# Performance work log

Hardware: AMD Instinct MI355X
Metric: run time of the kernel (lower is better)

The kernel has to match this reference:

```python
import jax, jax.numpy as jnp
import numpy as np

B = 4
N_SAMPLES = 32768
N_EVENTS = 32
N_HARMONICS = 16
SAMPLES_PER_FRAME = 256
N_FRAMES = N_SAMPLES // SAMPLES_PER_FRAME  # 128
SAMPLERATE = 22050
NYQ = SAMPLERATE // 2
MIN_F = 20.0 / NYQ
MAX_F = 4000.0 / NYQ
RES_BASE = 0.8
N_ROOMS = 8
LOG_SQRT_2PI = 0.5 * np.log(2.0 * np.pi).astype(np.float32)


def max_norm(x):
    return x / (jnp.max(jnp.abs(x), axis=-1, keepdims=True) + 1e-8)


def window(means, stds, n, mn, mx, eps=1e-8):
    # means/stds: [B, E, 1]; Normal pdf evaluated on linspace(0,1,n), max-normalized
    mu = mn + means * (mx - mn)
    sigma = eps + stds
    rng = jnp.linspace(0.0, 1.0, n, dtype=jnp.float32)[None, None, :]
    logp = -0.5 * ((rng - mu) / sigma) ** 2 - jnp.log(sigma) - LOG_SQRT_2PI
    return max_norm(jnp.exp(logp))


def interp_linear(x, out_size):
    # F.interpolate(mode='linear', align_corners=False) along last axis
    in_size = x.shape[-1]
    coords = (jnp.arange(out_size, dtype=jnp.float32) + 0.5) * (in_size / out_size) - 0.5
    coords = jnp.clip(coords, 0.0, in_size - 1.0)
    lo = jnp.floor(coords).astype(jnp.int32)
    hi = jnp.minimum(lo + 1, in_size - 1)
    w = (coords - lo.astype(jnp.float32))
    return x[..., lo] * (1.0 - w) + x[..., hi] * w


def fft_convolve(a, b):
    # zero-padded linear convolution via FFT, truncated to original length
    n = a.shape[-1]
    pa = jnp.pad(a, [(0, 0)] * (a.ndim - 1) + [(0, n)])
    pb = jnp.pad(b, [(0, 0)] * (b.ndim - 1) + [(0, n)])
    out = jnp.fft.irfft(jnp.fft.rfft(pa) * jnp.fft.rfft(pb), n=2 * n)
    return out[..., :n]


def setup_inputs():
    key = jax.random.key(0)
    k1, k2, k3, k4, k5 = jax.random.split(key, 5)
    return {
        'event_params': jax.random.uniform(k1, (B, N_EVENTS, N_HARMONICS + 6), dtype=jnp.float32),
        'mx_raw': jax.random.normal(k2, (B,), dtype=jnp.float32),
        'room_logits': jax.random.normal(k3, (B, N_ROOMS), dtype=jnp.float32),
        'noise': jax.random.uniform(k4, (1, 1, N_SAMPLES), dtype=jnp.float32, minval=-1.0, maxval=1.0),
        'impulse_responses': jax.random.normal(k5, (N_ROOMS, N_SAMPLES), dtype=jnp.float32) * 0.01,
    }


def reference(event_params, mx_raw, room_logits, noise, impulse_responses):
    b = event_params.shape[0]
    ep = event_params  # [B, E, 22], already in [0,1] (post-activation)
    freq_means = ep[:, :, 0:1] ** 2
    freq_stds = ep[:, :, 1:2] * 0.1
    time_means = ep[:, :, 2:3]
    time_stds = ep[:, :, 3:4] * 0.1
    f0 = ep[:, :, 4:5] ** 2
    amps = ep[:, :, 5:6] ** 2
    res = ep[:, :, 6:] * (1.0 - RES_BASE) + RES_BASE  # [B, E, H]
    mx = jax.nn.sigmoid(mx_raw).reshape(b, 1, 1)
    rooms = jax.nn.softmax(room_logits, axis=-1)

    # --- BandLimitedNoise ---
    nfft = N_SAMPLES // 2 + 1
    win = window(freq_means, freq_stds, nfft, MIN_F, MAX_F)  # [B, E, nfft]
    noise_spec = jnp.fft.rfft(noise, norm='ortho')            # [1, 1, nfft]
    bl_noise = jnp.fft.irfft(noise_spec * win, n=N_SAMPLES, norm='ortho')  # [B, E, N]

    # --- impulse (time) windows ---
    events = window(time_means, time_stds, N_SAMPLES, 0.0, 1.0)  # [B, E, N]

    # --- Resonance ---
    factors = jnp.arange(1, N_HARMONICS + 1, dtype=jnp.float32)
    f0s = MIN_F + (MAX_F - MIN_F) * f0                 # [B, E, 1]
    freqs = f0s * factors                               # [B, E, H]
    freqs = jnp.where(freqs >= 1.0, 0.0, freqs)
    freqs_fr = jnp.broadcast_to(freqs[..., None], freqs.shape + (N_FRAMES,))
    freqs_s = interp_linear(freqs_fr, N_SAMPLES)        # [B, E, H, N]
    res_fr = jnp.cumprod(jnp.broadcast_to(res[..., None], res.shape + (N_FRAMES,)), axis=-1)
    res_s = interp_linear(res_fr, N_SAMPLES)            # [B, E, H, N]
    resonances = jnp.sum(res_s * jnp.sin(jnp.cumsum(freqs_s * (2.0 * np.pi), axis=-1)), axis=2)  # [B, E, N]

    # --- locate events + resonance convolution (noise_coeff = 1) ---
    located = bl_noise * events * amps
    located = fft_convolve(located, resonances) + located
    located = jnp.sum(located, axis=1, keepdims=True)   # [B, 1, N]

    # --- reverb: rooms-weighted impulse response, dry/wet mix ---
    dry = located
    imp = jnp.einsum('br,rn->bn', rooms, impulse_responses)[:, None, :]
    wet = fft_convolve(located, imp)
    return dry * (1.0 - mx) + wet * mx
```

## Files before the change

kernel.cpp:

```cpp
#include <hip/hip_runtime.h>
#include <math.h>

#define NSAMP 32768
#define NPAD  65536
#define NCH   128
#define TWO_PI 6.2831853071795864f
#define MINF ((float)(20.0/11025.0))
#define DRF  ((float)(4000.0/11025.0 - 20.0/11025.0))

__device__ __forceinline__ float2 cxmul(float2 a, float2 b){
    return make_float2(a.x*b.x - a.y*b.y, a.x*b.y + a.y*b.x);
}

template<int DIR>
__device__ __forceinline__ void fft4v(float2* v, int i0, int i1, int i2, int i3){
    float2 a=v[i0], b=v[i1], c=v[i2], d=v[i3];
    float2 t0 = make_float2(a.x+c.x, a.y+c.y);
    float2 t1 = make_float2(a.x-c.x, a.y-c.y);
    float2 t2 = make_float2(b.x+d.x, b.y+d.y);
    float2 t3 = make_float2(b.x-d.x, b.y-d.y);
    v[i0] = make_float2(t0.x+t2.x, t0.y+t2.y);
    v[i2] = make_float2(t0.x-t2.x, t0.y-t2.y);
    if (DIR < 0) {
        v[i1] = make_float2(t1.x + t3.y, t1.y - t3.x);
        v[i3] = make_float2(t1.x - t3.y, t1.y + t3.x);
    } else {
        v[i1] = make_float2(t1.x - t3.y, t1.y + t3.x);
        v[i3] = make_float2(t1.x + t3.y, t1.y - t3.x);
    }
}

template<int DIR>
__device__ __forceinline__ void twm(float2& v, float c, float s){
    float sy = (DIR<0) ? -s : s;
    v = cxmul(v, make_float2(c, sy));
}

template<int DIR>
__device__ __forceinline__ void fft16r(float2* v){
    const float C1=0.92387953251128674f, S1=0.38268343236508978f, H=0.70710678118654752f;
    fft4v<DIR>(v,0,4,8,12);
    fft4v<DIR>(v,1,5,9,13);
    fft4v<DIR>(v,2,6,10,14);
    fft4v<DIR>(v,3,7,11,15);
    twm<DIR>(v[5],  C1, S1);
    twm<DIR>(v[6],  H,  H);
    twm<DIR>(v[7],  S1, C1);
    twm<DIR>(v[9],  H,  H);
    twm<DIR>(v[10], 0.0f, 1.0f);
    twm<DIR>(v[11], -H, H);
    twm<DIR>(v[13], S1, C1);
    twm<DIR>(v[14], -H, H);
    twm<DIR>(v[15], -C1, -S1);
    fft4v<DIR>(v,0,1,2,3);
    fft4v<DIR>(v,4,5,6,7);
    fft4v<DIR>(v,8,9,10,11);
    fft4v<DIR>(v,12,13,14,15);
}

template<int DIR>
__device__ __forceinline__ void fft8r(float2* v){
    const float H=0.70710678118654752f;
    #pragma unroll
    for (int n1=0;n1<4;n1++){
        float2 t=v[n1], u=v[n1+4];
        v[n1]   = make_float2(t.x+u.x, t.y+u.y);
        v[n1+4] = make_float2(t.x-u.x, t.y-u.y);
    }
    twm<DIR>(v[5], H, H);
    twm<DIR>(v[6], 0.0f, 1.0f);
    twm<DIR>(v[7], -H, H);
    fft4v<DIR>(v,0,1,2,3);
    fft4v<DIR>(v,4,5,6,7);
}

__device__ __forceinline__ int slot16(int r){ return ((r&3)<<2)|(r>>2); }
__device__ __forceinline__ int slot8(int r){ return ((r&1)<<2)|(r>>1); }
__device__ __forceinline__ int lxs(int l){ return l ^ ((l>>4)&15); }

template<int R>
__device__ __forceinline__ void twiddle(float2* v, float ang1){
    float s,c; __sincosf(ang1,&s,&c);
    float2 w[R];
    w[1] = make_float2(c,s);
    #pragma unroll
    for (int r=2;r<R;r++) w[r] = cxmul(w[r>>1], w[r-(r>>1)]);
    #pragma unroll
    for (int r=1;r<R;r++) v[r] = cxmul(v[r], w[r]);
}

template<int DIR>
__device__ __forceinline__ void n1_tail(float2 (&v)[16], float2* lds, int t, int p,
                                        float2* __restrict__ out)
{
    fft16r<DIR>(v);
    #pragma unroll
    for (int r=0;r<16;r++) lds[lxs(256*(t>>4) + 16*(t&15) + r)] = v[slot16(r)];
    __syncthreads();
    #pragma unroll
    for (int q=0;q<16;q++) v[q] = lds[lxs(256*q + t)];
    int jm = t & 15;
    if (jm) twiddle<16>(v, (DIR<0?-TWO_PI:TWO_PI)*(float)jm*(1.0f/256.0f));
    fft16r<DIR>(v);
    int j2 = 256*p + t;
    float2* yo = out + (j2>>4)*256 + (j2&15);
    #pragma unroll
    for (int r=0;r<16;r++) yo[16*r] = v[slot16(r)];
}

__global__ __launch_bounds__(256) void mfk_n1_noise_setup(const float* __restrict__ noise,
        float2* __restrict__ dst, const float* __restrict__ EP,
        const float* __restrict__ MXR, const float* __restrict__ RL,
        float* __restrict__ chP, unsigned* __restrict__ chQ, float* __restrict__ chR,
        float* __restrict__ cum, float* __restrict__ mxA, float* __restrict__ rmA)
{
    __shared__ float2 lds[4096];
    int t = threadIdx.x, px = blockIdx.x;
    if (px >= 8){
        int q = (px-8)*256 + t;
        int c = q >> 4, h = q & 15;
        const float* P = EP + c*22;
        const float LSQ = (float)0.9189385332046727;
        float f0m = __fmul_rn(P[4],P[4]);
        float f0s = __fadd_rn(MINF, __fmul_rn(f0m, DRF));
        float fr  = __fmul_rn(f0s, (float)(h+1));
        if (fr >= 1.0f) fr = 0.0f;
        chQ[q] = (unsigned)(unsigned long long)((double)fr*4294967296.0 + 0.5);
        float rs = __fadd_rn(__fmul_rn(P[6+h],0.2f),0.8f);
        chR[q] = rs;
        float cp = rs;
        float* crow = cum + (size_t)q*128;
        for (int jj=0;jj<128;jj++){ crow[jj] = cp; cp = __fmul_rn(cp, rs); }
        if (h == 0){
            float fm  = __fmul_rn(P[0],P[0]);
            float fmu = __fadd_rn(MINF, __fmul_rn(fm, DRF));
            float fsg = 1e-8f + P[1]*0.1f;
            float fsi = 1.0f/fsg;
            int i0 = (int)floorf(fmu*16384.0f + 0.5f);
            i0 = min(max(i0,0),16384);
            float rg = (float)i0 * (1.0f/16384.0f);
            float tt = (rg - fmu)*fsi;
            float Lc = logf(fsg) + LSQ;
            float sc = expf(-Lc) / (expf(-0.5f*tt*tt - Lc) + 1e-8f);
            float tmu = P[2];
            float tsg = 1e-8f + P[3]*0.1f;
            float tsi = 1.0f/tsg;
            int i1 = (int)floorf(tmu*32767.0f + 0.5f);
            i1 = min(max(i1,0),32767);
            float rg1 = (float)((double)i1 * (1.0/32767.0));
            float tt1 = (rg1 - tmu)*tsi;
            float Lc1 = logf(tsg) + LSQ;
            float sc1 = expf(-Lc1) / (expf(-0.5f*tt1*tt1 - Lc1) + 1e-8f);
            float amp = P[5]*P[5];
            float* o = chP + c*8;
            o[0]=fmu; o[1]=fsi; o[2]=sc; o[3]=tmu; o[4]=tsi; o[5]=sc1; o[6]=amp; o[7]=0.f;
        }
        if (q < 4){
            int b = q;
            mxA[b] = 1.0f/(1.0f + expf(-MXR[b]));
            const float* rl = RL + b*8;
            float mx = rl[0];
            for (int r=1;r<8;r++) mx = fmaxf(mx, rl[r]);
            float sum=0.f;
            float e2[8];
            for (int r=0;r<8;r++){ e2[r]=expf(rl[r]-mx); sum+=e2[r]; }
            for (int r=0;r<8;r++) rmA[b*8+r] = e2[r]/sum;
        }
        return;
    }
    int p = px;
    int j = 128*(t>>4) + 16*p + (t&15);
    float2 v[16];
    #pragma unroll
    for (int r=0;r<16;r++) v[r] = make_float2(noise[j + 2048*r], 0.0f);
    n1_tail<-1>(v, lds, t, p, dst);
}

__global__ __launch_bounds__(256) void mfk_n1_specwin(const float2* __restrict__ nspec,
        const float* __restrict__ chP, float2* __restrict__ dst, int g0)
{
    __shared__ float2 lds[4096];
    int t = threadIdx.x, p = blockIdx.x, pr = blockIdx.y;
    int c0 = g0 + 2*pr;
    const float* A = chP + c0*8;
    const float* B = chP + (c0+1)*8;
    float a0=A[0], a1=A[1], a2=A[2], b0=B[0], b1=B[1], b2=B[2];
    int j = 128*(t>>4) + 16*p + (t&15);
    float2 v[16];
    #pragma unroll
    for (int r=0;r<16;r++){
        int k = j + 2048*r;
        int kw = (k <= 16384) ? k : (32768 - k);
        float rg = (float)kw * (1.0f/16384.0f);
        float t0 = (rg - a0)*a1;
        float w0 = expf(-0.5f*t0*t0)*a2;
        float t1 = (rg - b0)*b1;
        float w1 = expf(-0.5f*t1*t1)*b2;
        float2 N = nspec[k];
        v[r] = make_float2(N.x*w0 - N.y*w1, N.y*w0 + N.x*w1);
    }
    n1_tail<1>(v, lds, t, p, dst + (size_t)pr*NSAMP);
}

template<int DIR>
__device__ __forceinline__ void n2_stageC(const float2* __restrict__ x, float2* lds, int t, int p)
{
    float2 v[16];
    int j2 = 256*(t>>5) + 32*p + (t&31);
    #pragma unroll
    for (int r=0;r<16;r++) v[r] = x[j2 + 2048*r];
    int jm = 32*p + (t&31);
    if (jm) twiddle<16>(v, (DIR<0?-TWO_PI:TWO_PI)*(float)jm*(1.0f/4096.0f));
    fft16r<DIR>(v);
    #pragma unroll
    for (int r=0;r<16;r++) lds[lxs(256*r + t)] = v[slot16(r)];
    __syncthreads();
}

template<int DIR>
__device__ __forceinline__ int n2_stageD(float2* lds, int t, int p, int u, float2 (&w8)[8])
{
    int q = t + 256*u;
    int j3 = ((q>>5)<<8) + 32*p + (q&31);
    #pragma unroll
    for (int r3=0;r3<8;r3++) w8[r3] = lds[lxs(256*(q>>5) + 32*r3 + (q&31))];
    if (j3) twiddle<8>(w8, (DIR<0?-TWO_PI:TWO_PI)*(float)j3*(1.0f/32768.0f));
    fft8r<DIR>(w8);
    return j3;
}

__global__ __launch_bounds__(256) void mfk_n2_noise(const float2* __restrict__ src,
                                                    float2* __restrict__ dst)
{
    __shared__ float2 lds[4096];
    int t = threadIdx.x, p = blockIdx.x;
    n2_stageC<-1>(src, lds, t, p);
    #pragma unroll
    for (int u=0;u<2;u++){
        float2 w8[8];
        int j3 = n2_stageD<-1>(lds, t, p, u, w8);
        #pragma unroll
        for (int r=0;r<8;r++) dst[j3 + 4096*r] = w8[slot8(r)];
    }
}

__global__ __launch_bounds__(256) void mfk_n2_unpack(const float2* __restrict__ src,
        const float* __restrict__ chP, float* __restrict__ locraw, int g0)
{
    __shared__ float2 lds[4096];
    int t = threadIdx.x, p = blockIdx.x, pr = blockIdx.y;
    n2_stageC<1>(src + (size_t)pr*NSAMP, lds, t, p);
    int lc0 = 2*pr;
    const float* C0 = chP + (g0+lc0)*8;
    const float* C1 = chP + (g0+lc0+1)*8;
    float c03=C0[3], c04=C0[4], c05=C0[5], c06=C0[6];
    float c13=C1[3], c14=C1[4], c15=C1[5], c16=C1[6];
    #pragma unroll
    for (int u=0;u<2;u++){
        float2 w8[8];
        int j3 = n2_stageD<1>(lds, t, p, u, w8);
        #pragma unroll
        for (int r=0;r<8;r++){
            int n = j3 + 4096*r;
            float2 val = w8[slot8(r)];
            float rg = (float)((double)n * (1.0/32767.0));
            float tt0 = (rg - c03)*c04;
            float ew0 = expf(-0.5f*tt0*tt0)*c05;
            float tt1 = (rg - c13)*c14;
            float ew1 = expf(-0.5f*tt1*tt1)*c15;
            locraw[(size_t)lc0*NSAMP + n]     = val.x*(1.0f/32768.0f)*ew0*c06;
            locraw[(size_t)(lc0+1)*NSAMP + n] = val.y*(1.0f/32768.0f)*ew1*c16;
        }
    }
}

__global__ __launch_bounds__(256) void mfk_packZres_f01(const float* __restrict__ locraw,
        const unsigned* __restrict__ chQ, const float* __restrict__ chR,
        const float* __restrict__ cum, float2* __restrict__ dst, int g0)
{
    __shared__ float2 lds[4096];
    float* cumS = (float*)lds;
    unsigned* qS = (unsigned*)(cumS + 2048);
    float* rS = cumS + 2064;
    int t = threadIdx.x, p = blockIdx.x, lc = blockIdx.y;
    int cg = g0 + lc;
    const float* crow = cum + (size_t)cg*2048;
    #pragma unroll
    for (int i=0;i<8;i++) cumS[t + 256*i] = crow[t + 256*i];
    if (t < 16){ qS[t] = chQ[cg*16 + t]; rS[t] = chR[cg*16 + t]; }
    __syncthreads();
    int j = 256*(t>>4) + 16*p + (t&15);
    float co0 = ((float)j + 0.5f)*0.00390625f - 0.5f;
    float fl = floorf(co0);
    float wf = co0 - fl;
    int ilo = (int)fl;
    float acc[8];
    #pragma unroll
    for (int r=0;r<8;r++) acc[r] = 0.0f;
    if (j == 0) acc[0] = 1.0f;
    unsigned T1 = (unsigned)(j+1);
    #pragma unroll
    for (int hh=0; hh<16; hh++){
        unsigned qq = qS[hh];
        float rs = rS[hh];
        float rs2 = rs*rs, rs4 = rs2*rs2, rs8 = rs4*rs4, rs16 = rs8*rs8;
        float mix = fmaf(rs - 1.0f, wf, 1.0f);
        const float* cr = cumS + hh*128;
        unsigned bits = qq * T1;
        unsigned step = qq << 12;
        float e_cur = (ilo >= 0) ? cr[ilo] : cr[15];
        float env0  = (ilo >= 0) ? 0.0f : cr[0];
        #pragma unroll
        for (int r=0;r<8;r++){
            float env;
            if (r == 0 && ilo < 0) env = env0;
            else env = (ilo == 15 && r == 7) ? e_cur : e_cur*mix;
            float m = (float)bits * 2.3283064365386963e-10f;
            float sv; asm("v_sin_f32 %0, %1" : "=v"(sv) : "v"(m));
            acc[r] = fmaf(env, sv, acc[r]);
            bits += step;
            if (!(r == 0 && ilo < 0)) e_cur *= rs16;
        }
    }
    const float* la = locraw + (size_t)lc*NSAMP;
    float2 v[16];
    #pragma unroll
    for (int r=0;r<8;r++) v[r] = make_float2(la[j + 4096*r], acc[r]);
    #pragma unroll
    for (int r=8;r<16;r++) v[r] = make_float2(0.f,0.f);
    __syncthreads();
    n1_tail<-1>(v, lds, t, p, dst + (size_t)lc*NPAD);
}

template<int DIR, int NSTORE>
__global__ __launch_bounds__(256) void mfk_f23(const float2* __restrict__ src,
                                               float2* __restrict__ dst)
{
    __shared__ float2 lds[4096];
    int t = threadIdx.x, p = blockIdx.x;
    size_t boff = (size_t)blockIdx.y * NPAD;
    int a = t>>4, w = t&15;
    int j = 256*a + 16*p + w;
    const float2* x = src + boff;
    float2 v[16];
    #pragma unroll
    for (int r=0;r<16;r++) v[r] = x[j + 4096*r];
    int jm = 16*p + w;
    if (jm) twiddle<16>(v, (DIR<0?-TWO_PI:TWO_PI)*(float)jm*(1.0f/4096.0f));
    fft16r<DIR>(v);
    #pragma unroll
    for (int r=0;r<16;r++) lds[lxs(256*a + 16*r + w)] = v[slot16(r)];
    __syncthreads();
    #pragma unroll
    for (int q=0;q<16;q++) v[q] = lds[lxs(256*q + t)];
    if (j) twiddle<16>(v, (DIR<0?-TWO_PI:TWO_PI)*(float)j*(1.0f/65536.0f));
    fft16r<DIR>(v);
    float2* yo = dst + boff + j;
    #pragma unroll
    for (int r=0;r<NSTORE;r++) yo[4096*r] = v[slot16(r)];
}

__global__ __launch_bounds__(256) void mfk_prodacc(const float2* __restrict__ Z,
        float2* __restrict__ T, int g0, int G, int addTo)
{
    int x = blockIdx.x;
    int beta = blockIdx.y;
    int z = blockIdx.z;
    int g = ((x>>4)<<3) | (x&7);
    int kb = (x&8) ? (255 - g) : g;
    int k = kb*256 + threadIdx.x;
    int km = (NPAD - k) & (NPAD-1);
    int cstart = max(64*beta + 32*z, g0);
    int cend   = min(64*beta + 32*z + 32, g0+G);
    float2 S0 = make_float2(0.f,0.f), S1 = make_float2(0.f,0.f);
    #pragma unroll 4
    for (int c=cstart; c<cend; ++c){
        const float2* zp = Z + (size_t)(c-g0)*NPAD;
        float2 a = zp[k], am = zp[km];
        float2 A0 = make_float2(0.5f*(a.x+am.x), 0.5f*(a.y-am.y));
        float2 R0 = make_float2(0.5f*(a.y+am.y), -0.5f*(a.x-am.x));
        float2 P = cxmul(A0,R0);
        if ((c>>5)&1){ S1.x += P.x; S1.y += P.y; }
        else         { S0.x += P.x; S0.y += P.y; }
    }
    const float s = 1.0f/65536.0f;
    float2 q = make_float2((S0.x - S1.y)*s, (S0.y + S1.x)*s);
    size_t idx = ((size_t)z*2 + beta)*NPAD + k;
    if (addTo){ float2 o = T[idx]; q.x += o.x; q.y += o.y; }
    T[idx] = q;
}

__global__ __launch_bounds__(256) void mfk_plain_f01(const float2* __restrict__ T,
        float2* __restrict__ dst)
{
    __shared__ float2 lds[4096];
    int t = threadIdx.x, p = blockIdx.x, b = blockIdx.y;
    const float2* x0 = T + (size_t)b*NPAD;
    const float2* x1 = T + (size_t)(2+b)*NPAD;
    int j = 256*(t>>4) + 16*p + (t&15);
    float2 v[16];
    #pragma unroll
    for (int r=0;r<16;r++){
        float2 u0 = x0[j + 4096*r], u1 = x1[j + 4096*r];
        v[r] = make_float2(u0.x+u1.x, u0.y+u1.y);
    }
    n1_tail<1>(v, lds, t, p, dst + (size_t)b*NPAD);
}

__global__ __launch_bounds__(256) void mfk_dry_f01(const float2* __restrict__ U2,
        const float* __restrict__ rmA, const float* __restrict__ IR, float2* __restrict__ dst)
{
    __shared__ float2 lds[4096];
    int t = threadIdx.x, p = blockIdx.x, b = blockIdx.y;
    int j = 256*(t>>4) + 16*p + (t&15);
    float rm[8];
    #pragma unroll
    for (int r=0;r<8;r++) rm[r] = rmA[b*8+r];
    const float2* Ub = U2 + (size_t)(b>>1)*NPAD;
    float2 v[16];
    #pragma unroll
    for (int r=0;r<8;r++){
        int n = j + 4096*r;
        float2 lcv = Ub[n];
        float locv = (b&1) ? lcv.y : lcv.x;
        float iv = 0.f;
        #pragma unroll
        for (int q=0;q<8;q++) iv += rm[q]*IR[(size_t)q*NSAMP + n];
        v[r] = make_float2(locv, iv);
    }
    #pragma unroll
    for (int r=8;r<16;r++) v[r] = make_float2(0.f,0.f);
    n1_tail<-1>(v, lds, t, p, dst + (size_t)b*NPAD);
}

__global__ __launch_bounds__(256) void mfk_prod_f01(const float2* __restrict__ Z,
        float2* __restrict__ dst)
{
    __shared__ float2 lds[4096];
    int t = threadIdx.x;
    int px = blockIdx.x;
    int p = (px < 8) ? px : 23 - px;
    int pr = blockIdx.y;
    const float2* z0 = Z + (size_t)(2*pr)*NPAD;
    const float2* z1 = z0 + NPAD;
    int j = 256*(t>>4) + 16*p + (t&15);
    float2 v[16];
    #pragma unroll
    for (int r=0;r<16;r++){
        int k = j + 4096*r;
        int km = (NPAD - k) & (NPAD-1);
        float2 a = z0[k], am = z0[km];
        float2 A0 = make_float2(0.5f*(a.x+am.x), 0.5f*(a.y-am.y));
        float2 R0 = make_float2(0.5f*(a.y+am.y), -0.5f*(a.x-am.x));
        float2 P0 = cxmul(A0,R0);
        float2 b = z1[k], bm = z1[km];
        float2 A1 = make_float2(0.5f*(b.x+bm.x), 0.5f*(b.y-bm.y));
        float2 R1 = make_float2(0.5f*(b.y+bm.y), -0.5f*(b.x-bm.x));
        float2 P1 = cxmul(A1,R1);
        const float s = 1.0f/65536.0f;
        v[r] = make_float2((P0.x - P1.y)*s, (P0.y + P1.x)*s);
    }
    n1_tail<1>(v, lds, t, p, dst + (size_t)pr*NPAD);
}

__global__ __launch_bounds__(256) void mfk_f23_final(const float2* __restrict__ src,
        const float2* __restrict__ U2, const float* __restrict__ mxA,
        float* __restrict__ out)
{
    __shared__ float2 lds[4096];
    int t = threadIdx.x, p = blockIdx.x;
    int pr = blockIdx.y;
    size_t boff = (size_t)pr * NPAD;
    int a = t>>4, w = t&15;
    int j = 256*a + 16*p + w;
    const float2* x = src + boff;
    float2 v[16];
    #pragma unroll
    for (int r=0;r<16;r++) v[r] = x[j + 4096*r];
    int jm = 16*p + w;
    if (jm) twiddle<16>(v, TWO_PI*(float)jm*(1.0f/4096.0f));
    fft16r<1>(v);
    #pragma unroll
    for (int r=0;r<16;r++) lds[lxs(256*a + 16*r + w)] = v[slot16(r)];
    __syncthreads();
    #pragma unroll
    for (int q=0;q<16;q++) v[q] = lds[lxs(256*q + t)];
    if (j) twiddle<16>(v, TWO_PI*(float)j*(1.0f/65536.0f));
    fft16r<1>(v);
    int b0 = 2*pr, b1 = b0+1;
    float mx0 = mxA[b0], mx1 = mxA[b1];
    const float2* Ub = U2 + (size_t)pr*NPAD;
    #pragma unroll
    for (int r=0;r<8;r++){
        int ts = j + 4096*r;
        float2 val = v[slot16(r)];
        float2 dry = Ub[ts];
        out[(size_t)b0*NSAMP+ts] = dry.x*(1.f-mx0) + val.x*mx0;
        out[(size_t)b1*NSAMP+ts] = dry.y*(1.f-mx1) + val.y*mx1;
    }
}

extern "C" void kernel_launch(void* const* d_in, const int* in_sizes, int n_in,
                              void* d_out, int out_size, void* d_ws, size_t ws_size,
                              hipStream_t stream)
{
    (void)in_sizes; (void)n_in; (void)out_size;
    const float* EP   = (const float*)d_in[0];
    const float* MXR  = (const float*)d_in[1];
    const float* RL   = (const float*)d_in[2];
    const float* NOISE= (const float*)d_in[3];
    const float* IR   = (const float*)d_in[4];
    float* out = (float*)d_out;
    char* w = (char*)d_ws;

    auto need = [](long long g)->long long {
        return 2LL*g*NPAD*8 + 1LL*g*NSAMP*4 + (long long)NSAMP*8
             + 2048LL*128*4 + (128LL*8 + 2048 + 2048 + 4 + 32)*4
             + 4LL*NPAD*8  + 2LL*NPAD*8  + 16384;
    };
    int G = 128;
    while (G > 4 && need(G) > (long long)ws_size) G >>= 1;

    size_t off = 0;
    auto alloc = [&](size_t bytes)->char* {
        char* p = w + off; off += (bytes + 255) & ~(size_t)255; return p;
    };
    float2*   arA    = (float2*)alloc((size_t)G*NPAD*8);
    float2*   arB    = (float2*)alloc((size_t)G*NPAD*8);
    float*    locraw = (float*) alloc((size_t)G*NSAMP*4);
    float2*   T      = (float2*)alloc(4LL*NPAD*8);
    float2*   U2     = (float2*)alloc(2LL*NPAD*8);
    float2*   nspec  = (float2*)alloc((size_t)NSAMP*8);
    float*    cum    = (float*) alloc(2048LL*128*4);
    float*    chP    = (float*) alloc(128*8*4);
    unsigned* chQ    = (unsigned*)alloc(2048*4);
    float*    chR    = (float*) alloc(2048*4);
    float*    mxA    = (float*) alloc(4*4);
    float*    rmA    = (float*) alloc(32*4);

    mfk_n1_noise_setup<<<dim3(16),256,0,stream>>>(NOISE, arB, EP, MXR, RL,
                                                  chP, chQ, chR, cum, mxA, rmA);
    mfk_n2_noise<<<dim3(8),256,0,stream>>>(arB, nspec);

    for (int g0 = 0; g0 < NCH; g0 += G){
        int P = G/2;
        mfk_n1_specwin<<<dim3(8,P),256,0,stream>>>(nspec, chP, arA, g0);
        mfk_n2_unpack<<<dim3(8,P),256,0,stream>>>(arA, chP, locraw, g0);
        mfk_packZres_f01<<<dim3(16,G),256,0,stream>>>(locraw, chQ, chR, cum, arA, g0);
        mfk_f23<-1,16><<<dim3(16,G),256,0,stream>>>(arA, arB);
        mfk_prodacc<<<dim3(256,2,2),256,0,stream>>>(arB, T, g0, G, (g0>0)?1:0);
    }

    mfk_plain_f01<<<dim3(16,2),256,0,stream>>>(T, arB);
    mfk_f23<1,8><<<dim3(16,2),256,0,stream>>>(arB, U2);

    mfk_dry_f01<<<dim3(16,4),256,0,stream>>>(U2, rmA, IR, arA);
    mfk_f23<-1,16><<<dim3(16,4),256,0,stream>>>(arA, arB);
    mfk_prod_f01<<<dim3(16,2),256,0,stream>>>(arB, arA);
    mfk_f23_final<<<dim3(16,2),256,0,stream>>>(arA, U2, mxA, out);
}
```

Before: 176.3 us.

## Fold impulse-response FFT into event-batch FFT launches and shrink reverb tail

The room-weighted impulse responses are now built and forward-transformed as two extra rows in the per-chunk pack/FFT launches, instead of in a separate tail stage. The reverb tail then forward-transforms only the two packed located signals and multiplies them against the precomputed IR spectra, halving the tail FFT grid. This moves serial tail work into an already wide launch to shorten the critical path. In exchange, workspace grows by two rows, and if G is smaller than the channel count the IR rows are recomputed in every chunk.

```diff
diff --git a/kernel.cpp b/kernel.cpp
--- a/kernel.cpp
+++ b/kernel.cpp
@@ -276,20 +276,44 @@
 
 __global__ __launch_bounds__(256) void mfk_packZres_f01(const float* __restrict__ locraw,
         const unsigned* __restrict__ chQ, const float* __restrict__ chR,
-        const float* __restrict__ cum, float2* __restrict__ dst, int g0)
-{
-    __shared__ float2 lds[4096];
+        const float* __restrict__ cum, const float* __restrict__ rmA,
+        const float* __restrict__ IR, float2* __restrict__ dst, int g0, int nev)
+{
+    __shared__ float2 lds[4096];
+    int t = threadIdx.x, p = blockIdx.x, lc = blockIdx.y;
+    int j = 256*(t>>4) + 16*p + (t&15);
+    if (lc >= nev){
+        int pi = lc - nev;
+        float rm0[8], rm1[8];
+        #pragma unroll
+        for (int q=0;q<8;q++){ rm0[q] = rmA[(2*pi)*8+q]; rm1[q] = rmA[(2*pi+1)*8+q]; }
+        float2 v[16];
+        #pragma unroll
+        for (int r=0;r<8;r++){
+            int n = j + 4096*r;
+            float i0 = 0.f, i1 = 0.f;
+            #pragma unroll
+            for (int q=0;q<8;q++){
+                float ir = IR[(size_t)q*NSAMP + n];
+                i0 = fmaf(rm0[q], ir, i0);
+                i1 = fmaf(rm1[q], ir, i1);
+            }
+            v[r] = make_float2(i0, i1);
+        }
+        #pragma unroll
+        for (int r=8;r<16;r++) v[r] = make_float2(0.f,0.f);
+        n1_tail<-1>(v, lds, t, p, dst + (size_t)lc*NPAD);
+        return;
+    }
     float* cumS = (float*)lds;
     unsigned* qS = (unsigned*)(cumS + 2048);
     float* rS = cumS + 2064;
-    int t = threadIdx.x, p = blockIdx.x, lc = blockIdx.y;
     int cg = g0 + lc;
     const float* crow = cum + (size_t)cg*2048;
     #pragma unroll
     for (int i=0;i<8;i++) cumS[t + 256*i] = crow[t + 256*i];
     if (t < 16){ qS[t] = chQ[cg*16 + t]; rS[t] = chR[cg*16 + t]; }
     __syncthreads();
-    int j = 256*(t>>4) + 16*p + (t&15);
     float co0 = ((float)j + 0.5f)*0.00390625f - 0.5f;
     float fl = floorf(co0);
     float wf = co0 - fl;
@@ -407,58 +431,47 @@
     n1_tail<1>(v, lds, t, p, dst + (size_t)b*NPAD);
 }
 
-__global__ __launch_bounds__(256) void mfk_dry_f01(const float2* __restrict__ U2,
-        const float* __restrict__ rmA, const float* __restrict__ IR, float2* __restrict__ dst)
-{
-    __shared__ float2 lds[4096];
-    int t = threadIdx.x, p = blockIdx.x, b = blockIdx.y;
+__global__ __launch_bounds__(256) void mfk_wet_f01(const float2* __restrict__ U2,
+        float2* __restrict__ dst)
+{
+    __shared__ float2 lds[4096];
+    int t = threadIdx.x, p = blockIdx.x, pr = blockIdx.y;
+    const float2* x = U2 + (size_t)pr*NPAD;
     int j = 256*(t>>4) + 16*p + (t&15);
-    float rm[8];
-    #pragma unroll
-    for (int r=0;r<8;r++) rm[r] = rmA[b*8+r];
-    const float2* Ub = U2 + (size_t)(b>>1)*NPAD;
-    float2 v[16];
-    #pragma unroll
-    for (int r=0;r<8;r++){
-        int n = j + 4096*r;
-        float2 lcv = Ub[n];
-        float locv = (b&1) ? lcv.y : lcv.x;
-        float iv = 0.f;
-        #pragma unroll
-        for (int q=0;q<8;q++) iv += rm[q]*IR[(size_t)q*NSAMP + n];
-        v[r] = make_float2(locv, iv);
-    }
+    float2 v[16];
+    #pragma unroll
+    for (int r=0;r<8;r++) v[r] = x[j + 4096*r];
     #pragma unroll
     for (int r=8;r<16;r++) v[r] = make_float2(0.f,0.f);
-    n1_tail<-1>(v, lds, t, p, dst + (size_t)b*NPAD);
-}
-
-__global__ __launch_bounds__(256) void mfk_prod_f01(const float2* __restrict__ Z,
-        float2* __restrict__ dst)
+    n1_tail<-1>(v, lds, t, p, dst + (size_t)pr*NPAD);
+}
+
+__global__ __launch_bounds__(256) void mfk_wetprod_f01(const float2* __restrict__ Zl,
+        const float2* __restrict__ Zi, float2* __restrict__ dst)
 {
     __shared__ float2 lds[4096];
     int t = threadIdx.x;
     int px = blockIdx.x;
     int p = (px < 8) ? px : 23 - px;
     int pr = blockIdx.y;
-    const float2* z0 = Z + (size_t)(2*pr)*NPAD;
-    const float2* z1 = z0 + NPAD;
+    const float2* zl = Zl + (size_t)pr*NPAD;
+    const float2* zi = Zi + (size_t)pr*NPAD;
     int j = 256*(t>>4) + 16*p + (t&15);
     float2 v[16];
     #pragma unroll
     for (int r=0;r<16;r++){
         int k = j + 4096*r;
         int km = (NPAD - k) & (NPAD-1);
-        float2 a = z0[k], am = z0[km];
-        float2 A0 = make_float2(0.5f*(a.x+am.x), 0.5f*(a.y-am.y));
-        float2 R0 = make_float2(0.5f*(a.y+am.y), -0.5f*(a.x-am.x));
-        float2 P0 = cxmul(A0,R0);
-        float2 b = z1[k], bm = z1[km];
-        float2 A1 = make_float2(0.5f*(b.x+bm.x), 0.5f*(b.y-bm.y));
-        float2 R1 = make_float2(0.5f*(b.y+bm.y), -0.5f*(b.x-bm.x));
-        float2 P1 = cxmul(A1,R1);
+        float2 a = zl[k], am = zl[km];
+        float2 L0 = make_float2(0.5f*(a.x+am.x), 0.5f*(a.y-am.y));
+        float2 L1 = make_float2(0.5f*(a.y+am.y), -0.5f*(a.x-am.x));
+        float2 b = zi[k], bm = zi[km];
+        float2 I0 = make_float2(0.5f*(b.x+bm.x), 0.5f*(b.y-bm.y));
+        float2 I1 = make_float2(0.5f*(b.y+bm.y), -0.5f*(b.x-bm.x));
+        float2 W0 = cxmul(L0,I0);
+        float2 W1 = cxmul(L1,I1);
         const float s = 1.0f/65536.0f;
-        v[r] = make_float2((P0.x - P1.y)*s, (P0.y + P1.x)*s);
+        v[r] = make_float2((W0.x - W1.y)*s, (W0.y + W1.x)*s);
     }
     n1_tail<1>(v, lds, t, p, dst + (size_t)pr*NPAD);
 }
@@ -514,7 +527,7 @@
     char* w = (char*)d_ws;
 
     auto need = [](long long g)->long long {
-        return 2LL*g*NPAD*8 + 1LL*g*NSAMP*4 + (long long)NSAMP*8
+        return 2LL*(g+2)*NPAD*8 + 1LL*g*NSAMP*4 + (long long)NSAMP*8
              + 2048LL*128*4 + (128LL*8 + 2048 + 2048 + 4 + 32)*4
              + 4LL*NPAD*8  + 2LL*NPAD*8  + 16384;
     };
@@ -525,8 +538,8 @@
     auto alloc = [&](size_t bytes)->char* {
         char* p = w + off; off += (bytes + 255) & ~(size_t)255; return p;
     };
-    float2*   arA    = (float2*)alloc((size_t)G*NPAD*8);
-    float2*   arB    = (float2*)alloc((size_t)G*NPAD*8);
+    float2*   arA    = (float2*)alloc((size_t)(G+2)*NPAD*8);
+    float2*   arB    = (float2*)alloc((size_t)(G+2)*NPAD*8);
     float*    locraw = (float*) alloc((size_t)G*NSAMP*4);
     float2*   T      = (float2*)alloc(4LL*NPAD*8);
     float2*   U2     = (float2*)alloc(2LL*NPAD*8);
@@ -546,16 +559,17 @@
         int P = G/2;
         mfk_n1_specwin<<<dim3(8,P),256,0,stream>>>(nspec, chP, arA, g0);
         mfk_n2_unpack<<<dim3(8,P),256,0,stream>>>(arA, chP, locraw, g0);
-        mfk_packZres_f01<<<dim3(16,G),256,0,stream>>>(locraw, chQ, chR, cum, arA, g0);
-        mfk_f23<-1,16><<<dim3(16,G),256,0,stream>>>(arA, arB);
+        mfk_packZres_f01<<<dim3(16,G+2),256,0,stream>>>(locraw, chQ, chR, cum,
+                                                        rmA, IR, arA, g0, G);
+        mfk_f23<-1,16><<<dim3(16,G+2),256,0,stream>>>(arA, arB);
         mfk_prodacc<<<dim3(256,2,2),256,0,stream>>>(arB, T, g0, G, (g0>0)?1:0);
     }
 
     mfk_plain_f01<<<dim3(16,2),256,0,stream>>>(T, arB);
     mfk_f23<1,8><<<dim3(16,2),256,0,stream>>>(arB, U2);
 
-    mfk_dry_f01<<<dim3(16,4),256,0,stream>>>(U2, rmA, IR, arA);
-    mfk_f23<-1,16><<<dim3(16,4),256,0,stream>>>(arA, arB);
-    mfk_prod_f01<<<dim3(16,2),256,0,stream>>>(arB, arA);
+    mfk_wet_f01<<<dim3(16,2),256,0,stream>>>(U2, arA);
+    mfk_f23<-1,16><<<dim3(16,2),256,0,stream>>>(arA, arB);
+    mfk_wetprod_f01<<<dim3(16,2),256,0,stream>>>(arB, arB + (size_t)G*NPAD, arA);
     mfk_f23_final<<<dim3(16,2),256,0,stream>>>(arA, U2, mxA, out);
 }
```

After: 180.2 us. +2.2%, slower.
